# Kernel tuning notes

Hardware: AMD Instinct MI355X
Metric: run time of the kernel (lower is better)

## Reference

```python
import jax, jax.numpy as jnp
import numpy as np

N, E, F, H, A, C, NC, L, AH = 50000, 800000, 768, 256, 128, 128, 7, 2, 4

def _ln(x, g, b):
    m = jnp.mean(x, axis=-1, keepdims=True)
    v = jnp.var(x, axis=-1, keepdims=True)
    return (x - m) / jnp.sqrt(v + 1e-5) * g + b

def setup_inputs() -> dict:
    key = jax.random.key(0)
    ks = jax.random.split(key, 32)
    s = 0.02
    d = {}
    d['x'] = jax.random.normal(ks[0], (N, F), jnp.float32)
    d['edge_index'] = jax.random.randint(ks[1], (2, E), 0, N, jnp.int32)
    d['W_in'] = jax.random.normal(ks[2], (F, H), jnp.float32) * s
    d['b_in'] = jnp.zeros((H,), jnp.float32)
    d['gin_W1'] = jax.random.normal(ks[3], (L, H, H), jnp.float32) * s
    d['gin_b1'] = jnp.zeros((L, H), jnp.float32)
    d['gin_lng'] = jnp.ones((L, H), jnp.float32)
    d['gin_lnb'] = jnp.zeros((L, H), jnp.float32)
    d['gin_W2'] = jax.random.normal(ks[4], (L, H, H), jnp.float32) * s
    d['gin_b2'] = jnp.zeros((L, H), jnp.float32)
    d['eps'] = jnp.zeros((L,), jnp.float32)
    d['ln_g'] = jnp.ones((L, H), jnp.float32)
    d['ln_b'] = jnp.zeros((L, H), jnp.float32)
    d['att_W1'] = jax.random.normal(ks[5], (AH, H, A), jnp.float32) * s
    d['att_b1'] = jnp.zeros((AH, A), jnp.float32)
    d['att_W2'] = jax.random.normal(ks[6], (AH, A), jnp.float32) * s
    d['att_b2'] = jnp.zeros((AH,), jnp.float32)
    d['Wc1'] = jax.random.normal(ks[7], (H, C), jnp.float32) * s
    d['bc1'] = jnp.zeros((C,), jnp.float32)
    d['lnc1_g'] = jnp.ones((C,), jnp.float32)
    d['lnc1_b'] = jnp.zeros((C,), jnp.float32)
    d['Wc2'] = jax.random.normal(ks[8], (C, C // 2), jnp.float32) * s
    d['bc2'] = jnp.zeros((C // 2,), jnp.float32)
    d['lnc2_g'] = jnp.ones((C // 2,), jnp.float32)
    d['lnc2_b'] = jnp.zeros((C // 2,), jnp.float32)
    d['Wc3'] = jax.random.normal(ks[9], (C // 2, NC), jnp.float32) * s
    d['bc3'] = jnp.zeros((NC,), jnp.float32)
    return d

def reference(x, edge_index, W_in, b_in, gin_W1, gin_b1, gin_lng, gin_lnb, gin_W2, gin_b2, eps, ln_g, ln_b, att_W1, att_b1, att_W2, att_b2, Wc1, bc1, lnc1_g, lnc1_b, Wc2, bc2, lnc2_g, lnc2_b, Wc3, bc3):
    src, dst = edge_index[0], edge_index[1]
    # input projection (use_residual and input_dim != gnn_hidden)
    h = x @ W_in + b_in  # [N,H]
    for i in range(L):
        agg = jax.ops.segment_sum(h[src], dst, num_segments=N)  # GIN sum aggregation
        m = (1.0 + eps[i]) * h + agg
        m = _ln(m @ gin_W1[i] + gin_b1[i], gin_lng[i], gin_lnb[i])
        m = jax.nn.relu(m) @ gin_W2[i] + gin_b2[i]
        hn = jax.nn.relu(_ln(m, ln_g[i], ln_b[i]))
        h = hn + h  # residual (shapes match)
    # multi-head attention pooling, softmax over node dim
    s = jnp.tanh(jnp.einsum('nd,kda->kna', h, att_W1) + att_b1[:, None, :])  # [AH,N,A]
    logits = jnp.einsum('kna,ka->kn', s, att_W2) + att_b2[:, None]  # [AH,N]
    a = jax.nn.softmax(logits, axis=1)  # [AH,N]
    z = jnp.einsum('kn,nd->kd', a, h)  # [AH,H]
    z_agg = jnp.mean(z, axis=0)  # [H]
    attn = a.T  # [N,AH]
    # classifier (full variant)
    c = jax.nn.relu(_ln(z_agg @ Wc1 + bc1, lnc1_g, lnc1_b))
    c = jax.nn.relu(_ln(c @ Wc2 + bc2, lnc2_g, lnc2_b))
    probs = jax.nn.softmax(c @ Wc3 + bc3, axis=0)
    return probs, attn
```

## Files before the change

### kernel.cpp

```cpp
#include <hip/hip_runtime.h>
#include <math.h>

#define NN 50000
#define NE 800000
#define FF 768
#define HH 256

typedef __attribute__((ext_vector_type(8))) short short8;
typedef __attribute__((ext_vector_type(4))) float f32x4;

__device__ inline unsigned short f2bf(float f) {
  unsigned u = __float_as_uint(f);
  u = u + 0x7fffu + ((u >> 16) & 1u);
  return (unsigned short)(u >> 16);
}

__global__ void k_count(const int* __restrict__ dstv, int* __restrict__ deg) {
  int e = blockIdx.x * 256 + threadIdx.x;
  if (e < NE) atomicAdd(&deg[dstv[e]], 1);
}

__global__ void k_scan(const int* __restrict__ deg, int* __restrict__ rowptr) {
  __shared__ int buf[1024];
  __shared__ int carry;
  int tid = threadIdx.x;
  if (tid == 0) { carry = 0; rowptr[0] = 0; }
  __syncthreads();
  for (int base = 0; base < NN; base += 1024) {
    int i = base + tid;
    int v = (i < NN) ? deg[i] : 0;
    buf[tid] = v;
    __syncthreads();
    for (int off = 1; off < 1024; off <<= 1) {
      int t = (tid >= off) ? buf[tid - off] : 0;
      __syncthreads();
      buf[tid] += t;
      __syncthreads();
    }
    int incl = buf[tid] + carry;
    if (i < NN) rowptr[i + 1] = incl;
    __syncthreads();
    if (tid == 1023) carry = incl;
    __syncthreads();
  }
}

__global__ void k_scatter(const int* __restrict__ srcv, const int* __restrict__ dstv,
                          int* __restrict__ cursor, int* __restrict__ csr_src) {
  int e = blockIdx.x * 256 + threadIdx.x;
  if (e < NE) {
    int d = dstv[e];
    int pos = atomicAdd(&cursor[d], 1);
    csr_src[pos] = srcv[e];
  }
}

__global__ void k_agg(const float* __restrict__ h, const int* __restrict__ rowptr,
                      const int* __restrict__ csr_src, const float* __restrict__ eps,
                      int layer, unsigned short* __restrict__ mb) {
  int node = (blockIdx.x * blockDim.x + threadIdx.x) >> 6;
  int lane = threadIdx.x & 63;
  if (node >= NN) return;
  int beg = rowptr[node], end = rowptr[node + 1];
  const float4* hv = (const float4*)h;
  float4 acc = make_float4(0.f, 0.f, 0.f, 0.f);
  for (int e = beg; e < end; ++e) {
    int s = csr_src[e];
    float4 v = hv[(size_t)s * 64 + lane];
    acc.x += v.x; acc.y += v.y; acc.z += v.z; acc.w += v.w;
  }
  float ep = 1.0f + eps[layer];
  float4 h0 = hv[(size_t)node * 64 + lane];
  acc.x += ep * h0.x; acc.y += ep * h0.y; acc.z += ep * h0.z; acc.w += ep * h0.w;
  ushort4 o;
  o.x = f2bf(acc.x); o.y = f2bf(acc.y); o.z = f2bf(acc.z); o.w = f2bf(acc.w);
  *(ushort4*)&mb[(size_t)node * 256 + lane * 4] = o;
}

__global__ void k_tcast(const float* __restrict__ src, unsigned short* __restrict__ dst,
                        int R, int C) {
  __shared__ float tile[32][33];
  int bx = blockIdx.x * 32, by = blockIdx.y * 32;
  int tx = threadIdx.x & 31, ty = threadIdx.x >> 5;
  for (int i = 0; i < 32; i += 8) {
    int r = by + ty + i, c = bx + tx;
    tile[ty + i][tx] = (r < R && c < C) ? src[(size_t)r * C + c] : 0.f;
  }
  __syncthreads();
  for (int i = 0; i < 32; i += 8) {
    int c = bx + ty + i, r = by + tx;
    if (c < C && r < R) dst[(size_t)c * R + r] = f2bf(tile[tx][ty + i]);
  }
}

template <int KTOT, int EPI, bool AF32>
__global__ __launch_bounds__(256) void k_mm(
    const void* __restrict__ Ap, const unsigned short* __restrict__ Bt,
    const float* __restrict__ bias, const float* __restrict__ g,
    const float* __restrict__ be, const float* __restrict__ resid,
    float* __restrict__ outf, unsigned short* __restrict__ outb) {
  __shared__ unsigned short As[64 * 40];
  __shared__ unsigned short Bs[256 * 40];
  __shared__ float redS[4][64];
  __shared__ float redQ[4][64];
  __shared__ float mvM[64], mvI[64];
  int t = threadIdx.x, lane = t & 63, wave = t >> 6;
  int row0 = blockIdx.x * 64;
  f32x4 acc[4][4];
#pragma unroll
  for (int i = 0; i < 4; i++)
#pragma unroll
    for (int j = 0; j < 4; j++) acc[i][j] = (f32x4)(0.f);
  int arow = t >> 2, ac = t & 3;
  int agr = row0 + arow; if (agr >= NN) agr = NN - 1;
  int m16 = lane & 15, kq = lane >> 4;

  for (int k0 = 0; k0 < KTOT; k0 += 32) {
    if (AF32) {
      const float* Af = (const float*)Ap + (size_t)agr * KTOT + k0 + ac * 8;
      float4 f0 = *(const float4*)Af;
      float4 f1 = *(const float4*)(Af + 4);
      short8 v;
      v[0] = (short)f2bf(f0.x); v[1] = (short)f2bf(f0.y);
      v[2] = (short)f2bf(f0.z); v[3] = (short)f2bf(f0.w);
      v[4] = (short)f2bf(f1.x); v[5] = (short)f2bf(f1.y);
      v[6] = (short)f2bf(f1.z); v[7] = (short)f2bf(f1.w);
      *(short8*)&As[arow * 40 + ac * 8] = v;
    } else {
      const unsigned short* Ab = (const unsigned short*)Ap + (size_t)agr * KTOT + k0 + ac * 8;
      *(float4*)&As[arow * 40 + ac * 8] = *(const float4*)Ab;
    }
#pragma unroll
    for (int it = 0; it < 4; it++) {
      int idx = t + it * 256;
      int br = idx >> 2, bc = idx & 3;
      *(float4*)&Bs[br * 40 + bc * 8] = *(const float4*)&Bt[(size_t)br * KTOT + k0 + bc * 8];
    }
    __syncthreads();
    short8 a[4], b[4];
#pragma unroll
    for (int rt = 0; rt < 4; rt++) a[rt] = *(const short8*)&As[(rt * 16 + m16) * 40 + kq * 8];
#pragma unroll
    for (int ct = 0; ct < 4; ct++)
      b[ct] = *(const short8*)&Bs[(wave * 64 + ct * 16 + m16) * 40 + kq * 8];
#pragma unroll
    for (int rt = 0; rt < 4; rt++)
#pragma unroll
      for (int ct = 0; ct < 4; ct++)
        acc[rt][ct] = __builtin_amdgcn_mfma_f32_16x16x32_bf16(a[rt], b[ct], acc[rt][ct], 0, 0, 0);
    __syncthreads();
  }

  int colbase = wave * 64 + m16;
  float bv[4];
#pragma unroll
  for (int ct = 0; ct < 4; ct++) bv[ct] = bias[colbase + ct * 16];

  if (EPI == 0) {
#pragma unroll
    for (int rt = 0; rt < 4; rt++)
#pragma unroll
      for (int reg = 0; reg < 4; reg++) {
        int r = row0 + rt * 16 + kq * 4 + reg;
        if (r < NN) {
#pragma unroll
          for (int ct = 0; ct < 4; ct++)
            outf[(size_t)r * 256 + colbase + ct * 16] = acc[rt][ct][reg] + bv[ct];
        }
      }
    return;
  }

  float s[4][4], q[4][4];
#pragma unroll
  for (int rt = 0; rt < 4; rt++)
#pragma unroll
    for (int reg = 0; reg < 4; reg++) { s[rt][reg] = 0.f; q[rt][reg] = 0.f; }
#pragma unroll
  for (int rt = 0; rt < 4; rt++)
#pragma unroll
    for (int ct = 0; ct < 4; ct++)
#pragma unroll
      for (int reg = 0; reg < 4; reg++) {
        float v = acc[rt][ct][reg] + bv[ct];
        acc[rt][ct][reg] = v;
        s[rt][reg] += v;
        q[rt][reg] += v * v;
      }
#pragma unroll
  for (int off = 1; off < 16; off <<= 1) {
#pragma unroll
    for (int rt = 0; rt < 4; rt++)
#pragma unroll
      for (int reg = 0; reg < 4; reg++) {
        s[rt][reg] += __shfl_xor(s[rt][reg], off, 64);
        q[rt][reg] += __shfl_xor(q[rt][reg], off, 64);
      }
  }
  if (m16 == 0) {
#pragma unroll
    for (int rt = 0; rt < 4; rt++)
#pragma unroll
      for (int reg = 0; reg < 4; reg++) {
        redS[wave][rt * 16 + kq * 4 + reg] = s[rt][reg];
        redQ[wave][rt * 16 + kq * 4 + reg] = q[rt][reg];
      }
  }
  __syncthreads();
  if (t < 64) {
    float ss = redS[0][t] + redS[1][t] + redS[2][t] + redS[3][t];
    float qq = redQ[0][t] + redQ[1][t] + redQ[2][t] + redQ[3][t];
    float mean = ss * (1.f / 256.f);
    float var = qq * (1.f / 256.f) - mean * mean;
    mvM[t] = mean;
    mvI[t] = rsqrtf(var + 1e-5f);
  }
  __syncthreads();
  float gv[4], bev[4];
#pragma unroll
  for (int ct = 0; ct < 4; ct++) { gv[ct] = g[colbase + ct * 16]; bev[ct] = be[colbase + ct * 16]; }
#pragma unroll
  for (int rt = 0; rt < 4; rt++)
#pragma unroll
    for (int reg = 0; reg < 4; reg++) {
      int rr = rt * 16 + kq * 4 + reg;
      int r = row0 + rr;
      if (r >= NN) continue;
      float mean = mvM[rr], inv = mvI[rr];
#pragma unroll
      for (int ct = 0; ct < 4; ct++) {
        int col = colbase + ct * 16;
        float val = fmaxf((acc[rt][ct][reg] - mean) * inv * gv[ct] + bev[ct], 0.f);
        if (EPI == 2) {
          val += resid[(size_t)r * 256 + col];
          outf[(size_t)r * 256 + col] = val;
        }
        outb[(size_t)r * 256 + col] = f2bf(val);
      }
    }
}

__global__ __launch_bounds__(256) void k_att(const unsigned short* __restrict__ hb,
    const unsigned short* __restrict__ W1T, const float* __restrict__ b1,
    const float* __restrict__ W2, const float* __restrict__ b2,
    float* __restrict__ logitsT) {
  __shared__ unsigned short As[64 * 40];
  __shared__ unsigned short Bs[128 * 40];
  __shared__ float redS[4][64];
  int t = threadIdx.x, lane = t & 63, wave = t >> 6;
  int kh = blockIdx.y;
  int row0 = blockIdx.x * 64;
  const unsigned short* Bt = W1T + (size_t)kh * 128 * 256;
  f32x4 acc[4][2];
#pragma unroll
  for (int i = 0; i < 4; i++)
#pragma unroll
    for (int j = 0; j < 2; j++) acc[i][j] = (f32x4)(0.f);
  int arow = t >> 2, ac = t & 3;
  int agr = row0 + arow; if (agr >= NN) agr = NN - 1;
  int m16 = lane & 15, kq = lane >> 4;
  for (int k0 = 0; k0 < 256; k0 += 32) {
    *(float4*)&As[arow * 40 + ac * 8] = *(const float4*)&hb[(size_t)agr * 256 + k0 + ac * 8];
#pragma unroll
    for (int it = 0; it < 2; it++) {
      int idx = t + it * 256;
      int br = idx >> 2, bc = idx & 3;
      *(float4*)&Bs[br * 40 + bc * 8] = *(const float4*)&Bt[(size_t)br * 256 + k0 + bc * 8];
    }
    __syncthreads();
    short8 a[4], b[2];
#pragma unroll
    for (int rt = 0; rt < 4; rt++) a[rt] = *(const short8*)&As[(rt * 16 + m16) * 40 + kq * 8];
#pragma unroll
    for (int ct = 0; ct < 2; ct++)
      b[ct] = *(const short8*)&Bs[(wave * 32 + ct * 16 + m16) * 40 + kq * 8];
#pragma unroll
    for (int rt = 0; rt < 4; rt++)
#pragma unroll
      for (int ct = 0; ct < 2; ct++)
        acc[rt][ct] = __builtin_amdgcn_mfma_f32_16x16x32_bf16(a[rt], b[ct], acc[rt][ct], 0, 0, 0);
    __syncthreads();
  }
  const float* b1k = b1 + kh * 128;
  const float* w2k = W2 + kh * 128;
  float b1v[2], w2v[2];
#pragma unroll
  for (int ct = 0; ct < 2; ct++) {
    int col = wave * 32 + ct * 16 + m16;
    b1v[ct] = b1k[col];
    w2v[ct] = w2k[col];
  }
  float p[4][4];
#pragma unroll
  for (int rt = 0; rt < 4; rt++)
#pragma unroll
    for (int reg = 0; reg < 4; reg++) p[rt][reg] = 0.f;
#pragma unroll
  for (int rt = 0; rt < 4; rt++)
#pragma unroll
    for (int ct = 0; ct < 2; ct++)
#pragma unroll
      for (int reg = 0; reg < 4; reg++)
        p[rt][reg] += tanhf(acc[rt][ct][reg] + b1v[ct]) * w2v[ct];
#pragma unroll
  for (int off = 1; off < 16; off <<= 1)
#pragma unroll
    for (int rt = 0; rt < 4; rt++)
#pragma unroll
      for (int reg = 0; reg < 4; reg++) p[rt][reg] += __shfl_xor(p[rt][reg], off, 64);
  if (m16 == 0) {
#pragma unroll
    for (int rt = 0; rt < 4; rt++)
#pragma unroll
      for (int reg = 0; reg < 4; reg++) redS[wave][rt * 16 + kq * 4 + reg] = p[rt][reg];
  }
  __syncthreads();
  if (t < 64) {
    int r = row0 + t;
    if (r < NN) {
      float sv = redS[0][t] + redS[1][t] + redS[2][t] + redS[3][t] + b2[kh];
      logitsT[(size_t)kh * NN + r] = sv;
    }
  }
}

__global__ void k_smax1(const float* __restrict__ logitsT, float* __restrict__ pmax,
                        float* __restrict__ psum) {
  int k = blockIdx.y;
  int tid = threadIdx.x;
  const float* L = logitsT + (size_t)k * NN;
  __shared__ float sm[256];
  float mx = -1e30f;
  for (int i = blockIdx.x * 256 + tid; i < NN; i += 128 * 256) mx = fmaxf(mx, L[i]);
  sm[tid] = mx; __syncthreads();
  for (int o = 128; o >= 1; o >>= 1) { if (tid < o) sm[tid] = fmaxf(sm[tid], sm[tid + o]); __syncthreads(); }
  float bmax = sm[0];
  __syncthreads();
  float s = 0.f;
  for (int i = blockIdx.x * 256 + tid; i < NN; i += 128 * 256) s += __expf(L[i] - bmax);
  sm[tid] = s; __syncthreads();
  for (int o = 128; o >= 1; o >>= 1) { if (tid < o) sm[tid] += sm[tid + o]; __syncthreads(); }
  if (tid == 0) { pmax[k * 128 + blockIdx.x] = bmax; psum[k * 128 + blockIdx.x] = sm[0]; }
}

__global__ void k_smax2(const float* __restrict__ pmax, const float* __restrict__ psum,
                        float* __restrict__ gs) {
  int k = blockIdx.x;
  int tid = threadIdx.x;
  __shared__ float sm[128], sv[128];
  float m = pmax[k * 128 + tid];
  sm[tid] = m; __syncthreads();
  for (int o = 64; o >= 1; o >>= 1) { if (tid < o) sm[tid] = fmaxf(sm[tid], sm[tid + o]); __syncthreads(); }
  float gm = sm[0];
  __syncthreads();
  sv[tid] = psum[k * 128 + tid] * __expf(m - gm);
  __syncthreads();
  for (int o = 64; o >= 1; o >>= 1) { if (tid < o) sv[tid] += sv[tid + o]; __syncthreads(); }
  if (tid == 0) { gs[k * 2] = gm; gs[k * 2 + 1] = sv[0]; }
}

__global__ void k_attnz(const float* __restrict__ logitsT, const float* __restrict__ gs,
                        const float* __restrict__ h, float* __restrict__ out_attn,
                        float* __restrict__ z) {
  int n0 = blockIdx.x * 128;
  int tid = threadIdx.x;
  __shared__ float a[4][128];
  for (int i = tid; i < 512; i += 256) {
    int k = i >> 7, n = i & 127;
    float v = 0.f;
    if (n0 + n < NN) v = __expf(logitsT[(size_t)k * NN + n0 + n] - gs[k * 2]) / gs[k * 2 + 1];
    a[k][n] = v;
  }
  __syncthreads();
  for (int i = tid; i < 512; i += 256) {
    int n = i >> 2, k = i & 3;
    if (n0 + n < NN) out_attn[(size_t)(n0 + n) * 4 + k] = a[k][n];
  }
  float z0 = 0.f, z1 = 0.f, z2 = 0.f, z3 = 0.f;
  int d = tid;
  int nmax = NN - n0; if (nmax > 128) nmax = 128;
  for (int n = 0; n < nmax; n++) {
    float hv = h[(size_t)(n0 + n) * 256 + d];
    z0 += a[0][n] * hv; z1 += a[1][n] * hv; z2 += a[2][n] * hv; z3 += a[3][n] * hv;
  }
  atomicAdd(&z[0 * 256 + d], z0);
  atomicAdd(&z[1 * 256 + d], z1);
  atomicAdd(&z[2 * 256 + d], z2);
  atomicAdd(&z[3 * 256 + d], z3);
}

__global__ void k_cls(const float* __restrict__ z, const float* __restrict__ Wc1,
                      const float* __restrict__ bc1, const float* __restrict__ g1,
                      const float* __restrict__ b1, const float* __restrict__ Wc2,
                      const float* __restrict__ bc2, const float* __restrict__ g2,
                      const float* __restrict__ b2, const float* __restrict__ Wc3,
                      const float* __restrict__ bc3, float* __restrict__ out) {
  int tid = threadIdx.x;
  __shared__ float za[256];
  __shared__ float buf[256];
  __shared__ float c1s[128];
  __shared__ float c2s[64];
  za[tid] = 0.25f * (z[tid] + z[256 + tid] + z[512 + tid] + z[768 + tid]);
  __syncthreads();
  float v1 = 0.f;
  if (tid < 128) {
    for (int d = 0; d < 256; d++) v1 += za[d] * Wc1[d * 128 + tid];
    v1 += bc1[tid];
  }
  buf[tid] = (tid < 128) ? v1 : 0.f; __syncthreads();
  for (int o = 128; o >= 1; o >>= 1) { if (tid < o) buf[tid] += buf[tid + o]; __syncthreads(); }
  float mean1 = buf[0] * (1.f / 128.f);
  __syncthreads();
  buf[tid] = (tid < 128) ? (v1 - mean1) * (v1 - mean1) : 0.f; __syncthreads();
  for (int o = 128; o >= 1; o >>= 1) { if (tid < o) buf[tid] += buf[tid + o]; __syncthreads(); }
  float inv1 = rsqrtf(buf[0] * (1.f / 128.f) + 1e-5f);
  __syncthreads();
  if (tid < 128) c1s[tid] = fmaxf((v1 - mean1) * inv1 * g1[tid] + b1[tid], 0.f);
  __syncthreads();
  float v2 = 0.f;
  if (tid < 64) {
    for (int d = 0; d < 128; d++) v2 += c1s[d] * Wc2[d * 64 + tid];
    v2 += bc2[tid];
  }
  buf[tid] = (tid < 64) ? v2 : 0.f; __syncthreads();
  for (int o = 128; o >= 1; o >>= 1) { if (tid < o) buf[tid] += buf[tid + o]; __syncthreads(); }
  float mean2 = buf[0] * (1.f / 64.f);
  __syncthreads();
  buf[tid] = (tid < 64) ? (v2 - mean2) * (v2 - mean2) : 0.f; __syncthreads();
  for (int o = 128; o >= 1; o >>= 1) { if (tid < o) buf[tid] += buf[tid + o]; __syncthreads(); }
  float inv2 = rsqrtf(buf[0] * (1.f / 64.f) + 1e-5f);
  __syncthreads();
  if (tid < 64) c2s[tid] = fmaxf((v2 - mean2) * inv2 * g2[tid] + b2[tid], 0.f);
  __syncthreads();
  if (tid < 7) {
    float l = 0.f;
    for (int d = 0; d < 64; d++) l += c2s[d] * Wc3[d * 7 + tid];
    buf[tid] = l + bc3[tid];
  }
  __syncthreads();
  if (tid == 0) {
    float mx = -1e30f;
    for (int i = 0; i < 7; i++) mx = fmaxf(mx, buf[i]);
    float s = 0.f;
    for (int i = 0; i < 7; i++) s += __expf(buf[i] - mx);
    for (int i = 0; i < 7; i++) out[i] = __expf(buf[i] - mx) / s;
  }
}

extern "C" void kernel_launch(void* const* d_in, const int* in_sizes, int n_in,
                              void* d_out, int out_size, void* d_ws, size_t ws_size,
                              hipStream_t stream) {
  const float* x       = (const float*)d_in[0];
  const int*   ei      = (const int*)d_in[1];
  const float* W_in    = (const float*)d_in[2];
  const float* b_in    = (const float*)d_in[3];
  const float* gin_W1  = (const float*)d_in[4];
  const float* gin_b1  = (const float*)d_in[5];
  const float* gin_lng = (const float*)d_in[6];
  const float* gin_lnb = (const float*)d_in[7];
  const float* gin_W2  = (const float*)d_in[8];
  const float* gin_b2  = (const float*)d_in[9];
  const float* eps     = (const float*)d_in[10];
  const float* ln_g    = (const float*)d_in[11];
  const float* ln_b    = (const float*)d_in[12];
  const float* att_W1  = (const float*)d_in[13];
  const float* att_b1  = (const float*)d_in[14];
  const float* att_W2  = (const float*)d_in[15];
  const float* att_b2  = (const float*)d_in[16];
  const float* Wc1     = (const float*)d_in[17];
  const float* bc1     = (const float*)d_in[18];
  const float* lnc1_g  = (const float*)d_in[19];
  const float* lnc1_b  = (const float*)d_in[20];
  const float* Wc2     = (const float*)d_in[21];
  const float* bc2     = (const float*)d_in[22];
  const float* lnc2_g  = (const float*)d_in[23];
  const float* lnc2_b  = (const float*)d_in[24];
  const float* Wc3     = (const float*)d_in[25];
  const float* bc3     = (const float*)d_in[26];
  float* out = (float*)d_out;
  (void)in_sizes; (void)n_in; (void)out_size; (void)ws_size;

  char* wsb = (char*)d_ws;
  size_t off = 0;
  auto alloc = [&](size_t bytes) {
    char* p = wsb + off;
    off += (bytes + 255) & ~(size_t)255;
    return p;
  };
  float*          h       = (float*)alloc((size_t)NN * HH * 4);
  unsigned short* hb      = (unsigned short*)alloc((size_t)NN * HH * 2);
  unsigned short* mb1     = (unsigned short*)alloc((size_t)NN * HH * 2);
  unsigned short* mb2     = (unsigned short*)alloc((size_t)NN * HH * 2);
  unsigned short* WinT    = (unsigned short*)alloc((size_t)HH * FF * 2);
  unsigned short* g1T     = (unsigned short*)alloc((size_t)2 * HH * HH * 2);
  unsigned short* g2T     = (unsigned short*)alloc((size_t)2 * HH * HH * 2);
  unsigned short* aW1T    = (unsigned short*)alloc((size_t)4 * 128 * HH * 2);
  float*          logitsT = (float*)alloc((size_t)4 * NN * 4);
  int*            deg     = (int*)alloc((size_t)NN * 4);
  int*            rowptr  = (int*)alloc((size_t)(NN + 1) * 4);
  int*            cursor  = (int*)alloc((size_t)NN * 4);
  int*            csr_src = (int*)alloc((size_t)NE * 4);
  float*          pmax    = (float*)alloc(4 * 128 * 4);
  float*          psum    = (float*)alloc(4 * 128 * 4);
  float*          gs      = (float*)alloc(8 * 4);
  float*          z       = (float*)alloc(4 * 256 * 4);

  const int* srcv = ei;
  const int* dstv = ei + NE;

  k_tcast<<<dim3((HH + 31) / 32, (FF + 31) / 32), 256, 0, stream>>>(W_in, WinT, FF, HH);
  for (int l = 0; l < 2; l++) {
    k_tcast<<<dim3(8, 8), 256, 0, stream>>>(gin_W1 + (size_t)l * HH * HH, g1T + (size_t)l * HH * HH, HH, HH);
    k_tcast<<<dim3(8, 8), 256, 0, stream>>>(gin_W2 + (size_t)l * HH * HH, g2T + (size_t)l * HH * HH, HH, HH);
  }
  for (int kh = 0; kh < 4; kh++)
    k_tcast<<<dim3(4, 8), 256, 0, stream>>>(att_W1 + (size_t)kh * HH * 128, aW1T + (size_t)kh * 128 * HH, HH, 128);

  hipMemsetAsync(deg, 0, (size_t)NN * 4, stream);
  hipMemsetAsync(z, 0, 4 * 256 * 4, stream);
  k_count<<<(NE + 255) / 256, 256, 0, stream>>>(dstv, deg);
  k_scan<<<1, 1024, 0, stream>>>(deg, rowptr);
  hipMemcpyAsync(cursor, rowptr, (size_t)NN * 4, hipMemcpyDeviceToDevice, stream);
  k_scatter<<<(NE + 255) / 256, 256, 0, stream>>>(srcv, dstv, cursor, csr_src);

  int gblocks = (NN + 63) / 64;
  k_mm<FF, 0, true><<<gblocks, 256, 0, stream>>>(x, WinT, b_in, nullptr, nullptr, nullptr, h, nullptr);

  for (int l = 0; l < 2; l++) {
    k_agg<<<(NN + 3) / 4, 256, 0, stream>>>(h, rowptr, csr_src, eps, l, mb1);
    k_mm<HH, 1, false><<<gblocks, 256, 0, stream>>>(mb1, g1T + (size_t)l * HH * HH,
        gin_b1 + l * HH, gin_lng + l * HH, gin_lnb + l * HH, nullptr, nullptr, mb2);
    k_mm<HH, 2, false><<<gblocks, 256, 0, stream>>>(mb2, g2T + (size_t)l * HH * HH,
        gin_b2 + l * HH, ln_g + l * HH, ln_b + l * HH, h, h, hb);
  }

  k_att<<<dim3(gblocks, 4), 256, 0, stream>>>(hb, aW1T, att_b1, att_W2, att_b2, logitsT);
  k_smax1<<<dim3(128, 4), 256, 0, stream>>>(logitsT, pmax, psum);
  k_smax2<<<4, 128, 0, stream>>>(pmax, psum, gs);
  k_attnz<<<(NN + 127) / 128, 256, 0, stream>>>(logitsT, gs, h, out + 7, z);
  k_cls<<<1, 256, 0, stream>>>(z, Wc1, bc1, lnc1_g, lnc1_b, Wc2, bc2, lnc2_g, lnc2_b,
                               Wc3, bc3, out);
}
```

Baseline: 977.6 us.

## Gather bf16 activations, fuse attention heads, parallelize degree scan

The GIN aggregation and attention pooling now read a bf16 copy of h instead of fp32. That copy is emitted by the input projection epilogue, and the fp32 write of h is skipped in the last layer. Together these roughly halve the gather traffic over 800k edges. The single-block scan becomes a per-thread chunked scan with wave shuffles in place of a 1024-step barrier loop. The attention kernel computes all 4 heads per block, with one wave per head, and replaces tanhf with an exp-based formula. These changes add bf16 rounding error to the aggregation and pooling inputs.

```diff
diff --git a/kernel.cpp b/kernel.cpp
--- a/kernel.cpp
+++ b/kernel.cpp
@@ -14,6 +14,9 @@
   u = u + 0x7fffu + ((u >> 16) & 1u);
   return (unsigned short)(u >> 16);
 }
+__device__ inline float bf2f(unsigned short b) {
+  return __uint_as_float(((unsigned)b) << 16);
+}
 
 __global__ void k_count(const int* __restrict__ dstv, int* __restrict__ deg) {
   int e = blockIdx.x * 256 + threadIdx.x;
@@ -21,27 +24,33 @@
 }
 
 __global__ void k_scan(const int* __restrict__ deg, int* __restrict__ rowptr) {
-  __shared__ int buf[1024];
-  __shared__ int carry;
+  const int CH = 49;
   int tid = threadIdx.x;
-  if (tid == 0) { carry = 0; rowptr[0] = 0; }
-  __syncthreads();
-  for (int base = 0; base < NN; base += 1024) {
-    int i = base + tid;
-    int v = (i < NN) ? deg[i] : 0;
-    buf[tid] = v;
-    __syncthreads();
-    for (int off = 1; off < 1024; off <<= 1) {
-      int t = (tid >= off) ? buf[tid - off] : 0;
-      __syncthreads();
-      buf[tid] += t;
-      __syncthreads();
-    }
-    int incl = buf[tid] + carry;
-    if (i < NN) rowptr[i + 1] = incl;
-    __syncthreads();
-    if (tid == 1023) carry = incl;
-    __syncthreads();
+  int lane = tid & 63, w = tid >> 6;
+  int base = tid * CH;
+  int sum = 0;
+  for (int i = 0; i < CH; i++) {
+    int idx = base + i;
+    if (idx < NN) sum += deg[idx];
+  }
+  int incl = sum;
+  for (int off = 1; off < 64; off <<= 1) {
+    int tv = __shfl_up(incl, off, 64);
+    if (lane >= off) incl += tv;
+  }
+  __shared__ int ws[16];
+  if (lane == 63) ws[w] = incl;
+  __syncthreads();
+  if (tid == 0) {
+    int c = 0;
+    for (int i = 0; i < 16; i++) { int tv = ws[i]; ws[i] = c; c += tv; }
+  }
+  __syncthreads();
+  int run = ws[w] + (incl - sum);
+  if (tid == 0) rowptr[0] = 0;
+  for (int i = 0; i < CH; i++) {
+    int idx = base + i;
+    if (idx < NN) { run += deg[idx]; rowptr[idx + 1] = run; }
   }
 }
 
@@ -55,25 +64,26 @@
   }
 }
 
-__global__ void k_agg(const float* __restrict__ h, const int* __restrict__ rowptr,
+__global__ void k_agg(const unsigned short* __restrict__ hb, const int* __restrict__ rowptr,
                       const int* __restrict__ csr_src, const float* __restrict__ eps,
                       int layer, unsigned short* __restrict__ mb) {
   int node = (blockIdx.x * blockDim.x + threadIdx.x) >> 6;
   int lane = threadIdx.x & 63;
   if (node >= NN) return;
   int beg = rowptr[node], end = rowptr[node + 1];
-  const float4* hv = (const float4*)h;
-  float4 acc = make_float4(0.f, 0.f, 0.f, 0.f);
+  const ushort4* hv = (const ushort4*)hb;
+  float ax = 0.f, ay = 0.f, az = 0.f, aw = 0.f;
   for (int e = beg; e < end; ++e) {
     int s = csr_src[e];
-    float4 v = hv[(size_t)s * 64 + lane];
-    acc.x += v.x; acc.y += v.y; acc.z += v.z; acc.w += v.w;
+    ushort4 v = hv[(size_t)s * 64 + lane];
+    ax += bf2f(v.x); ay += bf2f(v.y); az += bf2f(v.z); aw += bf2f(v.w);
   }
   float ep = 1.0f + eps[layer];
-  float4 h0 = hv[(size_t)node * 64 + lane];
-  acc.x += ep * h0.x; acc.y += ep * h0.y; acc.z += ep * h0.z; acc.w += ep * h0.w;
+  ushort4 h0 = hv[(size_t)node * 64 + lane];
+  ax += ep * bf2f(h0.x); ay += ep * bf2f(h0.y);
+  az += ep * bf2f(h0.z); aw += ep * bf2f(h0.w);
   ushort4 o;
-  o.x = f2bf(acc.x); o.y = f2bf(acc.y); o.z = f2bf(acc.z); o.w = f2bf(acc.w);
+  o.x = f2bf(ax); o.y = f2bf(ay); o.z = f2bf(az); o.w = f2bf(aw);
   *(ushort4*)&mb[(size_t)node * 256 + lane * 4] = o;
 }
 
@@ -93,7 +103,7 @@
   }
 }
 
-template <int KTOT, int EPI, bool AF32>
+template <int KTOT, int EPI, bool AF32, bool WF>
 __global__ __launch_bounds__(256) void k_mm(
     const void* __restrict__ Ap, const unsigned short* __restrict__ Bt,
     const float* __restrict__ bias, const float* __restrict__ g,
@@ -164,8 +174,11 @@
         int r = row0 + rt * 16 + kq * 4 + reg;
         if (r < NN) {
 #pragma unroll
-          for (int ct = 0; ct < 4; ct++)
-            outf[(size_t)r * 256 + colbase + ct * 16] = acc[rt][ct][reg] + bv[ct];
+          for (int ct = 0; ct < 4; ct++) {
+            float v = acc[rt][ct][reg] + bv[ct];
+            outf[(size_t)r * 256 + colbase + ct * 16] = v;
+            outb[(size_t)r * 256 + colbase + ct * 16] = f2bf(v);
+          }
         }
       }
     return;
@@ -233,7 +246,7 @@
         float val = fmaxf((acc[rt][ct][reg] - mean) * inv * gv[ct] + bev[ct], 0.f);
         if (EPI == 2) {
           val += resid[(size_t)r * 256 + col];
-          outf[(size_t)r * 256 + col] = val;
+          if (WF) outf[(size_t)r * 256 + col] = val;
         }
         outb[(size_t)r * 256 + col] = f2bf(val);
       }
@@ -245,63 +258,59 @@
     const float* __restrict__ W2, const float* __restrict__ b2,
     float* __restrict__ logitsT) {
   __shared__ unsigned short As[64 * 40];
-  __shared__ unsigned short Bs[128 * 40];
-  __shared__ float redS[4][64];
+  __shared__ unsigned short Bs[512 * 40];
   int t = threadIdx.x, lane = t & 63, wave = t >> 6;
-  int kh = blockIdx.y;
   int row0 = blockIdx.x * 64;
-  const unsigned short* Bt = W1T + (size_t)kh * 128 * 256;
-  f32x4 acc[4][2];
+  f32x4 acc[4][8];
 #pragma unroll
   for (int i = 0; i < 4; i++)
 #pragma unroll
-    for (int j = 0; j < 2; j++) acc[i][j] = (f32x4)(0.f);
+    for (int j = 0; j < 8; j++) acc[i][j] = (f32x4)(0.f);
   int arow = t >> 2, ac = t & 3;
   int agr = row0 + arow; if (agr >= NN) agr = NN - 1;
   int m16 = lane & 15, kq = lane >> 4;
   for (int k0 = 0; k0 < 256; k0 += 32) {
     *(float4*)&As[arow * 40 + ac * 8] = *(const float4*)&hb[(size_t)agr * 256 + k0 + ac * 8];
 #pragma unroll
-    for (int it = 0; it < 2; it++) {
+    for (int it = 0; it < 8; it++) {
       int idx = t + it * 256;
       int br = idx >> 2, bc = idx & 3;
-      *(float4*)&Bs[br * 40 + bc * 8] = *(const float4*)&Bt[(size_t)br * 256 + k0 + bc * 8];
+      *(float4*)&Bs[br * 40 + bc * 8] = *(const float4*)&W1T[(size_t)br * 256 + k0 + bc * 8];
     }
     __syncthreads();
-    short8 a[4], b[2];
+    short8 a[4];
 #pragma unroll
     for (int rt = 0; rt < 4; rt++) a[rt] = *(const short8*)&As[(rt * 16 + m16) * 40 + kq * 8];
 #pragma unroll
-    for (int ct = 0; ct < 2; ct++)
-      b[ct] = *(const short8*)&Bs[(wave * 32 + ct * 16 + m16) * 40 + kq * 8];
-#pragma unroll
-    for (int rt = 0; rt < 4; rt++)
-#pragma unroll
-      for (int ct = 0; ct < 2; ct++)
-        acc[rt][ct] = __builtin_amdgcn_mfma_f32_16x16x32_bf16(a[rt], b[ct], acc[rt][ct], 0, 0, 0);
+    for (int ct = 0; ct < 8; ct++) {
+      short8 b = *(const short8*)&Bs[(wave * 128 + ct * 16 + m16) * 40 + kq * 8];
+#pragma unroll
+      for (int rt = 0; rt < 4; rt++)
+        acc[rt][ct] = __builtin_amdgcn_mfma_f32_16x16x32_bf16(a[rt], b, acc[rt][ct], 0, 0, 0);
+    }
     __syncthreads();
   }
-  const float* b1k = b1 + kh * 128;
-  const float* w2k = W2 + kh * 128;
-  float b1v[2], w2v[2];
-#pragma unroll
-  for (int ct = 0; ct < 2; ct++) {
-    int col = wave * 32 + ct * 16 + m16;
-    b1v[ct] = b1k[col];
-    w2v[ct] = w2k[col];
-  }
+  const float* b1k = b1 + wave * 128;
+  const float* w2k = W2 + wave * 128;
   float p[4][4];
 #pragma unroll
   for (int rt = 0; rt < 4; rt++)
 #pragma unroll
     for (int reg = 0; reg < 4; reg++) p[rt][reg] = 0.f;
 #pragma unroll
-  for (int rt = 0; rt < 4; rt++)
-#pragma unroll
-    for (int ct = 0; ct < 2; ct++)
-#pragma unroll
-      for (int reg = 0; reg < 4; reg++)
-        p[rt][reg] += tanhf(acc[rt][ct][reg] + b1v[ct]) * w2v[ct];
+  for (int ct = 0; ct < 8; ct++) {
+    int col = ct * 16 + m16;
+    float b1v = b1k[col], w2v = w2k[col];
+#pragma unroll
+    for (int rt = 0; rt < 4; rt++)
+#pragma unroll
+      for (int reg = 0; reg < 4; reg++) {
+        float xv = acc[rt][ct][reg] + b1v;
+        xv = fminf(fmaxf(xv, -10.f), 10.f);
+        float ex = __expf(2.f * xv);
+        p[rt][reg] += (ex - 1.f) / (ex + 1.f) * w2v;
+      }
+  }
 #pragma unroll
   for (int off = 1; off < 16; off <<= 1)
 #pragma unroll
@@ -309,18 +318,14 @@
 #pragma unroll
       for (int reg = 0; reg < 4; reg++) p[rt][reg] += __shfl_xor(p[rt][reg], off, 64);
   if (m16 == 0) {
-#pragma unroll
-    for (int rt = 0; rt < 4; rt++)
-#pragma unroll
-      for (int reg = 0; reg < 4; reg++) redS[wave][rt * 16 + kq * 4 + reg] = p[rt][reg];
-  }
-  __syncthreads();
-  if (t < 64) {
-    int r = row0 + t;
-    if (r < NN) {
-      float sv = redS[0][t] + redS[1][t] + redS[2][t] + redS[3][t] + b2[kh];
-      logitsT[(size_t)kh * NN + r] = sv;
-    }
+    float b2v = b2[wave];
+#pragma unroll
+    for (int rt = 0; rt < 4; rt++)
+#pragma unroll
+      for (int reg = 0; reg < 4; reg++) {
+        int r = row0 + rt * 16 + kq * 4 + reg;
+        if (r < NN) logitsT[(size_t)wave * NN + r] = p[rt][reg] + b2v;
+      }
   }
 }
 
@@ -360,7 +365,7 @@
 }
 
 __global__ void k_attnz(const float* __restrict__ logitsT, const float* __restrict__ gs,
-                        const float* __restrict__ h, float* __restrict__ out_attn,
+                        const unsigned short* __restrict__ hb, float* __restrict__ out_attn,
                         float* __restrict__ z) {
   int n0 = blockIdx.x * 128;
   int tid = threadIdx.x;
@@ -380,7 +385,7 @@
   int d = tid;
   int nmax = NN - n0; if (nmax > 128) nmax = 128;
   for (int n = 0; n < nmax; n++) {
-    float hv = h[(size_t)(n0 + n) * 256 + d];
+    float hv = bf2f(hb[(size_t)(n0 + n) * 256 + d]);
     z0 += a[0][n] * hv; z1 += a[1][n] * hv; z2 += a[2][n] * hv; z3 += a[3][n] * hv;
   }
   atomicAdd(&z[0 * 256 + d], z0);
@@ -524,20 +529,24 @@
   k_scatter<<<(NE + 255) / 256, 256, 0, stream>>>(srcv, dstv, cursor, csr_src);
 
   int gblocks = (NN + 63) / 64;
-  k_mm<FF, 0, true><<<gblocks, 256, 0, stream>>>(x, WinT, b_in, nullptr, nullptr, nullptr, h, nullptr);
+  k_mm<FF, 0, true, true><<<gblocks, 256, 0, stream>>>(x, WinT, b_in, nullptr, nullptr, nullptr, h, hb);
 
   for (int l = 0; l < 2; l++) {
-    k_agg<<<(NN + 3) / 4, 256, 0, stream>>>(h, rowptr, csr_src, eps, l, mb1);
-    k_mm<HH, 1, false><<<gblocks, 256, 0, stream>>>(mb1, g1T + (size_t)l * HH * HH,
+    k_agg<<<(NN + 3) / 4, 256, 0, stream>>>(hb, rowptr, csr_src, eps, l, mb1);
+    k_mm<HH, 1, false, true><<<gblocks, 256, 0, stream>>>(mb1, g1T + (size_t)l * HH * HH,
         gin_b1 + l * HH, gin_lng + l * HH, gin_lnb + l * HH, nullptr, nullptr, mb2);
-    k_mm<HH, 2, false><<<gblocks, 256, 0, stream>>>(mb2, g2T + (size_t)l * HH * HH,
-        gin_b2 + l * HH, ln_g + l * HH, ln_b + l * HH, h, h, hb);
-  }
-
-  k_att<<<dim3(gblocks, 4), 256, 0, stream>>>(hb, aW1T, att_b1, att_W2, att_b2, logitsT);
+    if (l == 0)
+      k_mm<HH, 2, false, true><<<gblocks, 256, 0, stream>>>(mb2, g2T + (size_t)l * HH * HH,
+          gin_b2 + l * HH, ln_g + l * HH, ln_b + l * HH, h, h, hb);
+    else
+      k_mm<HH, 2, false, false><<<gblocks, 256, 0, stream>>>(mb2, g2T + (size_t)l * HH * HH,
+          gin_b2 + l * HH, ln_g + l * HH, ln_b + l * HH, h, nullptr, hb);
+  }
+
+  k_att<<<gblocks, 256, 0, stream>>>(hb, aW1T, att_b1, att_W2, att_b2, logitsT);
   k_smax1<<<dim3(128, 4), 256, 0, stream>>>(logitsT, pmax, psum);
   k_smax2<<<4, 128, 0, stream>>>(pmax, psum, gs);
-  k_attnz<<<(NN + 127) / 128, 256, 0, stream>>>(logitsT, gs, h, out + 7, z);
+  k_attnz<<<(NN + 127) / 128, 256, 0, stream>>>(logitsT, gs, hb, out + 7, z);
   k_cls<<<1, 256, 0, stream>>>(z, Wc1, bc1, lnc1_g, lnc1_b, Wc2, bc2, lnc2_g, lnc2_b,
                                Wc3, bc3, out);
 }
```

Result: faster. 956.3 us (-2.2%).
